# Kernel optimization log

Measured on AMD Instinct MI355X. Metric: run time of the kernel, lower is better.

## Reference

```python
import jax, jax.numpy as jnp
import numpy as np


def _gcn_conv(x, W, b, row, col, norm, n_nodes):
    # x: [N, Fin]; W: [Fin, Fout]. PyG GCNConv: linear -> normalized gather/scatter-add -> +bias
    h = x @ W                                   # [N, Fout]
    msgs = h[row] * norm[:, None]               # [E+N, Fout] gather + scale
    out = jax.ops.segment_sum(msgs, col, num_segments=n_nodes)  # scatter-add
    return out + b


def _gcn_norm(edge_index, n_nodes):
    # add self-loops, then sym-normalize: deg^{-1/2}[row] * deg^{-1/2}[col]
    loops = jnp.arange(n_nodes, dtype=edge_index.dtype)
    row = jnp.concatenate([edge_index[0], loops])
    col = jnp.concatenate([edge_index[1], loops])
    ones = jnp.ones(row.shape[0], dtype=jnp.float32)
    deg = jax.ops.segment_sum(ones, col, num_segments=n_nodes)
    dinv = jnp.where(deg > 0, jax.lax.rsqrt(deg), 0.0)
    norm = dinv[row] * dinv[col]
    return row, col, norm


def setup_inputs() -> dict:
    key = jax.random.key(0)
    k1, k2, k3, k4 = jax.random.split(key, 4)
    N, E, F, H, C = 100000, 1600000, 256, 128, 40
    x = jax.random.normal(k1, (N, F), dtype=jnp.float32)
    edge_index = jax.random.randint(k2, (2, E), 0, N, dtype=jnp.int64)
    W1 = jax.random.normal(k3, (F, H), dtype=jnp.float32) * (1.0 / np.sqrt(F))
    b1 = jnp.zeros((H,), dtype=jnp.float32)
    W2 = jax.random.normal(k4, (H, C), dtype=jnp.float32) * (1.0 / np.sqrt(H))
    b2 = jnp.zeros((C,), dtype=jnp.float32)
    return {"x": x, "edge_index": edge_index, "W1": W1, "b1": b1, "W2": W2, "b2": b2}


def reference(x, edge_index, W1, b1, W2, b2):
    n_nodes = x.shape[0]
    row, col, norm = _gcn_norm(edge_index, n_nodes)
    h = _gcn_conv(x, W1, b1, row, col, norm, n_nodes)
    h = jax.nn.relu(h)
    # F.dropout in eval mode is identity (reference run deterministically)
    h = _gcn_conv(h, W2, b2, row, col, norm, n_nodes)
    return jax.nn.log_softmax(h, axis=1)
```

## Files before the change

kernel.cpp:

```cpp
#include <hip/hip_runtime.h>
#include <hip/hip_bf16.h>
#include <math.h>
#include <stdint.h>

typedef unsigned short u16;
typedef unsigned int u32;
typedef __attribute__((ext_vector_type(8))) short short8;
typedef __attribute__((ext_vector_type(4))) float f32x4;
typedef __attribute__((ext_vector_type(2))) float f32x2;

#define BN 256
#define NBMAX 400
#define EPB 4096
#define ST1 160
#define ST2 192

__device__ __forceinline__ u16 bfbits(float f) {
    __hip_bfloat16 h = __float2bfloat16(f);
    return *reinterpret_cast<u16*>(&h);
}
__device__ __forceinline__ float bflo(u32 v) { return __uint_as_float(v << 16); }
__device__ __forceinline__ float bfhi(u32 v) { return __uint_as_float(v & 0xffff0000u); }

template <bool HI>
__device__ __forceinline__ f32x2 fp8pair(u32 v) {
#if __has_builtin(__builtin_amdgcn_cvt_pk_f32_fp8)
    return __builtin_amdgcn_cvt_pk_f32_fp8(v, HI);
#else
    f32x2 r;
    r.x = __builtin_amdgcn_cvt_f32_fp8(v, HI ? 2 : 0);
    r.y = __builtin_amdgcn_cvt_f32_fp8(v, HI ? 3 : 1);
    return r;
#endif
}

__device__ __forceinline__ int sigma128(int col) {
    int a = col >> 6, c = (col >> 4) & 3, lr = col & 15;
    return (a << 6) + (lr << 2) + c;
}

__global__ __launch_bounds__(256) void k_pre(const int* __restrict__ ei, int E, int n, int nb,
                                             int nblkc, int* __restrict__ gcnt,
                                             const float* __restrict__ w1, short* __restrict__ w1bf,
                                             const float* __restrict__ b1, const float* __restrict__ w2,
                                             float* __restrict__ b1p, float* __restrict__ w2p) {
    __shared__ int sh[NBMAX];
    const int t = threadIdx.x;
    const int b = blockIdx.x;
    if (b < nblkc) {
        const int* col = ei + E;
        for (int i = t; i < nb; i += 256) sh[i] = 0;
        __syncthreads();
        const int base = b * EPB;
#pragma unroll
        for (int j = 0; j < 16; ++j) {
            int e = base + j * 256 + t;
            if (e < E) {
                unsigned c = (unsigned)col[e];
                if (c < (unsigned)n) atomicAdd(&sh[c >> 8], 1);
            }
        }
        __syncthreads();
        for (int i = t; i < nb; i += 256)
            if (sh[i]) atomicAdd(&gcnt[i], sh[i]);
    } else if (b < nblkc + 128) {
        int i = (b - nblkc) * 256 + t;
        int e = i & 7, l = (i >> 3) & 63, kt = (i >> 9) & 7, ct = i >> 12;
        int k = kt * 32 + (l >> 4) * 8 + e;
        int c = ct * 16 + (l & 15);
        w1bf[i] = (short)bfbits(w1[(size_t)k * 128 + c]);
    } else {
        int i = (b - nblkc - 128) * 256 + t;
        if (i < 128) b1p[sigma128(i)] = b1[i];
        int j = i - 128;
        if (j >= 0 && j < 128 * 40) {
            int col = j / 40, jj = j - col * 40;
            w2p[sigma128(col) * 40 + jj] = w2[j];
        }
    }
}

__global__ __launch_bounds__(512) void k_bscan(const int* __restrict__ gcnt,
                                               int* __restrict__ ebase, int* __restrict__ cursor,
                                               int* __restrict__ off, int nb, int n) {
    __shared__ int sh[512];
    const int t = threadIdx.x;
    int v = (t < nb) ? gcnt[t] : 0;
    sh[t] = v;
    __syncthreads();
    for (int d = 1; d < 512; d <<= 1) {
        int x = (t >= d) ? sh[t - d] : 0;
        __syncthreads();
        sh[t] += x;
        __syncthreads();
    }
    if (t < nb) {
        int excl = sh[t] - v;
        ebase[t] = excl;
        cursor[t] = excl;
    }
    if (t == 0) {
        ebase[nb] = sh[511];
        off[n] = sh[511] + n;
    }
}

struct SMemScat { int cnt[NBMAX]; int cbase[NBMAX]; };
union SMemU {
    SMemScat s;
    u16 xt[64 * 128];
};

__global__ __launch_bounds__(256) void k_scatg1(const int* __restrict__ ei,
                                                int* __restrict__ cursor, u32* __restrict__ staging,
                                                int E, int n, int nb, int nblks,
                                                const float* __restrict__ x,
                                                const short* __restrict__ w1bf,
                                                u32* __restrict__ hbf8) {
    __shared__ SMemU sm;
    const int t = threadIdx.x;
    if ((int)blockIdx.x < nblks) {
        for (int i = t; i < nb; i += 256) sm.s.cnt[i] = 0;
        __syncthreads();
        const int base = blockIdx.x * EPB;
        int rr[16], cc[16], rk[16];
#pragma unroll
        for (int j = 0; j < 16; ++j) {
            int e = base + j * 256 + t;
            cc[j] = -1;
            if (e < E) {
                unsigned r = (unsigned)ei[e], c = (unsigned)ei[E + e];
                if (r < (unsigned)n && c < (unsigned)n) {
                    rr[j] = (int)r;
                    cc[j] = (int)c;
                    rk[j] = atomicAdd(&sm.s.cnt[c >> 8], 1);
                }
            }
        }
        __syncthreads();
        for (int i = t; i < nb; i += 256)
            if (sm.s.cnt[i]) sm.s.cbase[i] = atomicAdd(&cursor[i], sm.s.cnt[i]);
        __syncthreads();
#pragma unroll
        for (int j = 0; j < 16; ++j) {
            if (cc[j] >= 0) {
                int b = cc[j] >> 8;
                staging[sm.s.cbase[b] + rk[j]] = (u32)rr[j] | ((u32)(cc[j] & (BN - 1)) << 17);
            }
        }
        return;
    }
    const int bid = blockIdx.x - nblks;
    const int wv = t >> 6, l = t & 63;
    const int mrow = wv >> 1, mcol = wv & 1;
    const int lr = l & 15, kg = l >> 4;
    const int n0 = bid * 64;

    const short* bbase = w1bf + ((size_t)(4 * mcol) * 8) * 64 * 8 + (size_t)l * 8;

    f32x4 zero = {0.f, 0.f, 0.f, 0.f};
    f32x4 acc[2][4];
#pragma unroll
    for (int m = 0; m < 2; ++m)
#pragma unroll
        for (int c = 0; c < 4; ++c) acc[m][c] = zero;

#pragma unroll
    for (int p = 0; p < 2; ++p) {
        __syncthreads();
#pragma unroll
        for (int j = 0; j < 8; ++j) {
            int idx = j * 256 + t;
            int row = idx >> 5;
            int kf4 = idx & 31;
            int grow = n0 + row;
            if (grow > n - 1) grow = n - 1;
            float4 v = *(const float4*)(x + (size_t)grow * 256 + p * 128 + kf4 * 4);
            u32 w0 = (u32)bfbits(v.x) | ((u32)bfbits(v.y) << 16);
            u32 w1v = (u32)bfbits(v.z) | ((u32)bfbits(v.w) << 16);
            int bir = kf4 * 8;
            int sb = row * 256 + (bir ^ ((row & 7) << 4));
            *(uint2*)((char*)sm.xt + sb) = make_uint2(w0, w1v);
        }
        __syncthreads();
#pragma unroll
        for (int ktl = 0; ktl < 4; ++ktl) {
            int kt = p * 4 + ktl;
            short8 af[2];
#pragma unroll
            for (int m = 0; m < 2; ++m) {
                int r = 32 * mrow + 16 * m + lr;
                int bir = ktl * 64 + kg * 16;
                int sb = r * 256 + (bir ^ ((r & 7) << 4));
                af[m] = *(const short8*)((const char*)sm.xt + sb);
            }
#pragma unroll
            for (int c = 0; c < 4; ++c) {
                short8 bfrag = *(const short8*)(bbase + ((size_t)(c * 8 + kt) * 64) * 8);
#pragma unroll
                for (int m = 0; m < 2; ++m)
                    acc[m][c] = __builtin_amdgcn_mfma_f32_16x16x32_bf16(af[m], bfrag,
                                                                        acc[m][c], 0, 0, 0);
            }
        }
    }

#pragma unroll
    for (int m = 0; m < 2; ++m) {
        int rbase = n0 + 32 * mrow + 16 * m + kg * 4;
#pragma unroll
        for (int r = 0; r < 4; ++r) {
            int row = rbase + r;
            if (row < n) {
                int w = __builtin_amdgcn_cvt_pk_fp8_f32(acc[m][0][r], acc[m][1][r], 0, false);
                w = __builtin_amdgcn_cvt_pk_fp8_f32(acc[m][2][r], acc[m][3][r], w, true);
                hbf8[(size_t)row * 32 + 16 * mcol + lr] = (u32)w;
            }
        }
    }
}

__global__ __launch_bounds__(256) void k_build(const u32* __restrict__ staging,
                                               const int* __restrict__ ebase,
                                               int* __restrict__ csrs, int* __restrict__ off,
                                               float* __restrict__ dinv, int n) {
    __shared__ int sh[256];
    __shared__ int cur[256];
    const int t = threadIdx.x;
    const int b = blockIdx.x;
    const int e0 = ebase[b], e1 = ebase[b + 1];
    const int node0 = b * BN;
    const int nn = min(BN, n - node0);
    sh[t] = 0;
    __syncthreads();
    for (int i = e0 + t; i < e1; i += 256)
        atomicAdd(&sh[staging[i] >> 17], 1);
    __syncthreads();
    const int mycnt = sh[t];
    const int myval = (t < nn) ? mycnt + 1 : 0;
    sh[t] = myval;
    __syncthreads();
    for (int d = 1; d < 256; d <<= 1) {
        int x = (t >= d) ? sh[t - d] : 0;
        __syncthreads();
        sh[t] += x;
        __syncthreads();
    }
    const int excl = sh[t] - myval;
    const int csrbase = e0 + node0;
    if (t < nn) {
        int node = node0 + t;
        int o = csrbase + excl;
        off[node] = o;
        dinv[node] = rsqrtf((float)(mycnt + 1));
        csrs[o] = node;
        cur[t] = o + 1;
    }
    __syncthreads();
    for (int i = e0 + t; i < e1; i += 256) {
        u32 v = staging[i];
        int p = atomicAdd(&cur[v >> 17], 1);
        csrs[p] = (int)(v & 0x1FFFF);
    }
}

__global__ __launch_bounds__(256) void k_agg1(const u32* __restrict__ hbf8,
                                              const int* __restrict__ off,
                                              const int* __restrict__ csrs,
                                              const float* __restrict__ dinv,
                                              const float* __restrict__ b1p,
                                              u16* __restrict__ h1b, int n) {
    __shared__ int s_s[8][ST1];
    __shared__ float s_f[8][ST1];
    const int t = threadIdx.x, h = t >> 5, fl = t & 31;
    const int node = blockIdx.x * 8 + h;
    const int nd = node < n ? node : n - 1;
    const float dn = dinv[nd];
    const int e0 = off[nd], e1 = off[nd + 1];
    const int deg = e1 - e0;
    const int nst = deg < ST1 ? deg : ST1;
    for (int i = fl; i < nst; i += 32) {
        int s = csrs[e0 + i];
        s_s[h][i] = s;
        s_f[h][i] = dinv[s] * dn;
    }
    __syncthreads();

    const int onst = __shfl_xor(nst, 32, 64);
    const int nmin = nst < onst ? nst : onst;
    const int nmax = nst > onst ? nst : onst;
    const int odeg = __shfl_xor(deg, 32, 64);
    const int dmax = deg > odeg ? deg : odeg;

    const u32* hb = hbf8;
    float a0 = 0.f, a1 = 0.f, a2 = 0.f, a3 = 0.f;
    int i = 0;
    for (; i + 16 <= nmin; i += 16) {
        u32 vv[16];
        float ww[16];
#pragma unroll
        for (int k = 0; k < 16; ++k) {
            int s = s_s[h][i + k];
            ww[k] = s_f[h][i + k];
            vv[k] = hb[(size_t)s * 32 + fl];
        }
#pragma unroll
        for (int k = 0; k < 16; ++k) {
            f32x2 lo = fp8pair<false>(vv[k]), hi = fp8pair<true>(vv[k]);
            a0 = fmaf(lo.x, ww[k], a0); a1 = fmaf(lo.y, ww[k], a1);
            a2 = fmaf(hi.x, ww[k], a2); a3 = fmaf(hi.y, ww[k], a3);
        }
    }
    for (; i + 4 <= nmin; i += 4) {
        u32 vv[4];
        float ww[4];
#pragma unroll
        for (int k = 0; k < 4; ++k) {
            int s = s_s[h][i + k];
            ww[k] = s_f[h][i + k];
            vv[k] = hb[(size_t)s * 32 + fl];
        }
#pragma unroll
        for (int k = 0; k < 4; ++k) {
            f32x2 lo = fp8pair<false>(vv[k]), hi = fp8pair<true>(vv[k]);
            a0 = fmaf(lo.x, ww[k], a0); a1 = fmaf(lo.y, ww[k], a1);
            a2 = fmaf(hi.x, ww[k], a2); a3 = fmaf(hi.y, ww[k], a3);
        }
    }
    for (; i < nmin; ++i) {
        int s = s_s[h][i];
        float w = s_f[h][i];
        u32 v = hb[(size_t)s * 32 + fl];
        f32x2 lo = fp8pair<false>(v), hi = fp8pair<true>(v);
        a0 = fmaf(lo.x, w, a0); a1 = fmaf(lo.y, w, a1);
        a2 = fmaf(hi.x, w, a2); a3 = fmaf(hi.y, w, a3);
    }
    for (; i < nmax; ++i) {
        bool ok = i < nst;
        int s = ok ? s_s[h][i] : nd;
        float w = ok ? s_f[h][i] : 0.f;
        u32 v = hb[(size_t)s * 32 + fl];
        f32x2 lo = fp8pair<false>(v), hi = fp8pair<true>(v);
        a0 = fmaf(lo.x, w, a0); a1 = fmaf(lo.y, w, a1);
        a2 = fmaf(hi.x, w, a2); a3 = fmaf(hi.y, w, a3);
    }
    for (int j = ST1; j < dmax; ++j) {
        bool ok = j < deg;
        int s = ok ? csrs[e0 + j] : nd;
        float w = ok ? dinv[s] * dn : 0.f;
        u32 v = hb[(size_t)s * 32 + fl];
        f32x2 lo = fp8pair<false>(v), hi = fp8pair<true>(v);
        a0 = fmaf(lo.x, w, a0); a1 = fmaf(lo.y, w, a1);
        a2 = fmaf(hi.x, w, a2); a3 = fmaf(hi.y, w, a3);
    }

    float4 bb = *(const float4*)(b1p + 4 * fl);
    float r0 = fmaxf(a0 + bb.x, 0.f);
    float r1 = fmaxf(a1 + bb.y, 0.f);
    float r2 = fmaxf(a2 + bb.z, 0.f);
    float r3 = fmaxf(a3 + bb.w, 0.f);
    if (node < n) {
        uint2 o;
        o.x = (u32)bfbits(r0) | ((u32)bfbits(r1) << 16);
        o.y = (u32)bfbits(r2) | ((u32)bfbits(r3) << 16);
        ((uint2*)h1b)[(size_t)node * 32 + fl] = o;
    }
}

__global__ __launch_bounds__(64) void k_gemm2(const u16* __restrict__ h1b,
                                              const float* __restrict__ w2p,
                                              u32* __restrict__ h2q, float* __restrict__ scl,
                                              int n) {
    __shared__ float hs[64 * 132];
    const int t = threadIdx.x;
    const int n0 = blockIdx.x * 64;
    const uint4* src = (const uint4*)(h1b + (size_t)n0 * 128);
#pragma unroll
    for (int i = 0; i < 16; ++i) {
        int idx = i * 64 + t;
        int r = idx >> 4, q = idx & 15;
        uint4 v = make_uint4(0u, 0u, 0u, 0u);
        if (n0 + r < n) v = src[(size_t)r * 16 + q];
        *(float4*)&hs[r * 132 + q * 8] =
            make_float4(bflo(v.x), bfhi(v.x), bflo(v.y), bfhi(v.y));
        *(float4*)&hs[r * 132 + q * 8 + 4] =
            make_float4(bflo(v.z), bfhi(v.z), bflo(v.w), bfhi(v.w));
    }
    __syncthreads();

    float acc[40];
#pragma unroll
    for (int c = 0; c < 40; ++c) acc[c] = 0.f;

    for (int k4 = 0; k4 < 32; ++k4) {
        float4 hv = *(const float4*)&hs[t * 132 + 4 * k4];
#pragma unroll
        for (int j = 0; j < 4; ++j) {
            float xv = (j == 0) ? hv.x : (j == 1) ? hv.y : (j == 2) ? hv.z : hv.w;
            const float* wr = w2p + (size_t)(4 * k4 + j) * 40;
#pragma unroll
            for (int c = 0; c < 40; ++c) acc[c] = fmaf(xv, wr[c], acc[c]);
        }
    }
    __syncthreads();

    float mx = 0.f;
#pragma unroll
    for (int c = 0; c < 40; ++c) mx = fmaxf(mx, fabsf(acc[c]));
    const float qs = mx > 0.f ? 127.f / mx : 0.f;
    u32* rowp = (u32*)hs + t * 16;
#pragma unroll
    for (int j = 0; j < 10; ++j) {
        u32 w = 0;
#pragma unroll
        for (int k = 0; k < 4; ++k) {
            int q = __float2int_rn(acc[4 * j + k] * qs);
            q = q > 127 ? 127 : (q < -127 ? -127 : q);
            w |= ((u32)(q & 255)) << (8 * k);
        }
        rowp[j] = w;
    }
#pragma unroll
    for (int j = 10; j < 16; ++j) rowp[j] = 0;
    __syncthreads();
    const int nrow = (n - n0 < 64) ? n - n0 : 64;
    uint4* dst = (uint4*)(h2q + (size_t)n0 * 16);
    const uint4* s4 = (const uint4*)hs;
#pragma unroll
    for (int i = 0; i < 4; ++i) {
        int idx = i * 64 + t;
        if ((idx >> 2) < nrow) dst[idx] = s4[idx];
    }
    if (t < nrow) scl[n0 + t] = mx * (1.f / 127.f);
}

__global__ __launch_bounds__(256) void k_agg2(const u32* __restrict__ h2q,
                                              const float* __restrict__ scl,
                                              const int* __restrict__ off,
                                              const int* __restrict__ csrs,
                                              const float* __restrict__ dinv,
                                              const float* __restrict__ b2,
                                              float* __restrict__ out, int n) {
    __shared__ int s_s[4][ST2];
    __shared__ float s_f[4][ST2];
    const int t = threadIdx.x, wv = t >> 6, l = t & 63;
    const int node = blockIdx.x * 4 + wv;
    const int nd = node < n ? node : n - 1;
    const float dn = dinv[nd];
    const int e0 = off[nd], e1 = off[nd + 1];
    const int deg = e1 - e0;
    const int nst = deg < ST2 ? deg : ST2;
    for (int i = l; i < nst; i += 64) {
        int s = csrs[e0 + i];
        s_s[wv][i] = s;
        s_f[wv][i] = dinv[s] * dn * scl[s];
    }
    __syncthreads();

    const int g = l >> 4;
    const int fl = l & 15;

#define ACC4(v, w)                                                         \
    {                                                                      \
        a0 = fmaf((float)(int)(signed char)((v) & 0xff), (w), a0);         \
        a1 = fmaf((float)(int)(signed char)(((v) >> 8) & 0xff), (w), a1);  \
        a2 = fmaf((float)(int)(signed char)(((v) >> 16) & 0xff), (w), a2); \
        a3 = fmaf((float)(int)(signed char)((v) >> 24), (w), a3);          \
    }

    float a0 = 0.f, a1 = 0.f, a2 = 0.f, a3 = 0.f;
    int base = 0;
    for (; base + 16 <= nst; base += 16) {
        int eA = base + g, eB = base + 4 + g, eC = base + 8 + g, eD = base + 12 + g;
        int sA = s_s[wv][eA], sB = s_s[wv][eB], sC = s_s[wv][eC], sD = s_s[wv][eD];
        float wA = s_f[wv][eA], wB = s_f[wv][eB], wC = s_f[wv][eC], wD = s_f[wv][eD];
        u32 vA = h2q[(size_t)sA * 16 + fl];
        u32 vB = h2q[(size_t)sB * 16 + fl];
        u32 vC = h2q[(size_t)sC * 16 + fl];
        u32 vD = h2q[(size_t)sD * 16 + fl];
        ACC4(vA, wA); ACC4(vB, wB); ACC4(vC, wC); ACC4(vD, wD);
    }
    for (; base < nst; base += 4) {
        int e = base + g;
        bool ok = e < nst;
        int s = ok ? s_s[wv][e] : nd;
        float w = ok ? s_f[wv][e] : 0.f;
        u32 v = h2q[(size_t)s * 16 + fl];
        ACC4(v, w);
    }
    for (int j = nst; j < deg; j += 4) {
        int e = j + g;
        bool ok = e < deg;
        int s = ok ? csrs[e0 + e] : nd;
        float w = ok ? dinv[s] * dn * scl[s] : 0.f;
        u32 v = h2q[(size_t)s * 16 + fl];
        ACC4(v, w);
    }
#undef ACC4

    float t0 = __shfl(a0, (l + 32) & 63, 64);
    float t1 = __shfl(a1, (l + 32) & 63, 64);
    float t2 = __shfl(a2, (l + 32) & 63, 64);
    float t3 = __shfl(a3, (l + 32) & 63, 64);
    a0 += t0; a1 += t1; a2 += t2; a3 += t3;
    t0 = __shfl(a0, (l + 16) & 63, 64);
    t1 = __shfl(a1, (l + 16) & 63, 64);
    t2 = __shfl(a2, (l + 16) & 63, 64);
    t3 = __shfl(a3, (l + 16) & 63, 64);
    a0 += t0; a1 += t1; a2 += t2; a3 += t3;

    const bool act = (l < 10);
    float4 bb = *(const float4*)(b2 + 4 * (act ? l : 9));
    float v0 = a0 + bb.x, v1 = a1 + bb.y, v2 = a2 + bb.z, v3 = a3 + bb.w;

    float m = act ? fmaxf(fmaxf(v0, v1), fmaxf(v2, v3)) : -INFINITY;
#pragma unroll
    for (int d = 8; d > 0; d >>= 1) m = fmaxf(m, __shfl_xor(m, d, 16));
    float s = act ? (__expf(v0 - m) + __expf(v1 - m) + __expf(v2 - m) + __expf(v3 - m)) : 0.f;
#pragma unroll
    for (int d = 8; d > 0; d >>= 1) s += __shfl_xor(s, d, 16);
    float ls = logf(s);
    if (node < n && act) {
        float4 o = make_float4(v0 - m - ls, v1 - m - ls, v2 - m - ls, v3 - m - ls);
        *(float4*)(out + (size_t)node * 40 + 4 * l) = o;
    }
}

extern "C" void kernel_launch(void* const* d_in, const int* in_sizes, int n_in,
                              void* d_out, int out_size, void* d_ws, size_t ws_size,
                              hipStream_t stream) {
    const float* x = (const float*)d_in[0];
    const int* ei = (const int*)d_in[1];
    const float* w1 = (const float*)d_in[2];
    const float* b1 = (const float*)d_in[3];
    const float* w2 = (const float*)d_in[4];
    const float* b2 = (const float*)d_in[5];
    float* out = (float*)d_out;

    const int N = in_sizes[0] / 256;
    const int E = in_sizes[1] / 2;
    const int NB = (N + BN - 1) / BN;

    char* p = (char*)d_ws;
    auto alloc = [&](size_t bytes) {
        char* r = p;
        p += (bytes + 255) & ~(size_t)255;
        return r;
    };
    int* gcnt = (int*)alloc((size_t)NB * 4);
    int* ebase = (int*)alloc((size_t)(NB + 1) * 4);
    int* cursor = (int*)alloc((size_t)NB * 4);
    int* off = (int*)alloc((size_t)(N + 1) * 4);
    float* dinv = (float*)alloc((size_t)N * 4);
    float* scl = (float*)alloc((size_t)N * 4);
    int* csrs = (int*)alloc((size_t)(E + N) * 4);
    short* w1bf = (short*)alloc(32768 * 2);
    float* b1p = (float*)alloc(128 * 4);
    float* w2p = (float*)alloc(128 * 40 * 4);
    u32* hbf8 = (u32*)alloc((size_t)N * 32 * 4);
    u16* h1b = (u16*)alloc((size_t)N * 128 * 2);
    u32* staging = (u32*)h1b;
    u32* h2q = hbf8;

    const int nblk = (E + EPB - 1) / EPB;
    const int g1blk = (N + 63) / 64;

    (void)hipMemsetAsync(gcnt, 0, (size_t)NB * 4, stream);
    k_pre<<<nblk + 128 + 21, 256, 0, stream>>>(ei, E, N, NB, nblk, gcnt, w1, w1bf,
                                               b1, w2, b1p, w2p);
    k_bscan<<<1, 512, 0, stream>>>(gcnt, ebase, cursor, off, NB, N);
    k_scatg1<<<nblk + g1blk, 256, 0, stream>>>(ei, cursor, staging, E, N, NB, nblk,
                                               x, w1bf, hbf8);
    k_build<<<NB, 256, 0, stream>>>(staging, ebase, csrs, off, dinv, N);
    k_agg1<<<(N + 7) / 8, 256, 0, stream>>>(hbf8, off, csrs, dinv, b1p, h1b, N);
    k_gemm2<<<g1blk, 64, 0, stream>>>(h1b, w2p, h2q, scl, N);
    k_agg2<<<(N + 3) / 4, 256, 0, stream>>>(h2q, scl, off, csrs, dinv, b2, out, N);
}
```

Measured before the change: 237.5 us.

## Fuse second-layer GEMM and int8 quantization into first aggregation kernel

```diff
diff --git a/kernel.cpp b/kernel.cpp
--- a/kernel.cpp
+++ b/kernel.cpp
@@ -12,7 +12,7 @@
 #define BN 256
 #define NBMAX 400
 #define EPB 4096
-#define ST1 160
+#define ST1 152
 #define ST2 192
 
 __device__ __forceinline__ u16 bfbits(float f) {
@@ -43,7 +43,7 @@
                                              int nblkc, int* __restrict__ gcnt,
                                              const float* __restrict__ w1, short* __restrict__ w1bf,
                                              const float* __restrict__ b1, const float* __restrict__ w2,
-                                             float* __restrict__ b1p, float* __restrict__ w2p) {
+                                             float* __restrict__ b1p, float* __restrict__ w2t) {
     __shared__ int sh[NBMAX];
     const int t = threadIdx.x;
     const int b = blockIdx.x;
@@ -74,8 +74,8 @@
         if (i < 128) b1p[sigma128(i)] = b1[i];
         int j = i - 128;
         if (j >= 0 && j < 128 * 40) {
-            int col = j / 40, jj = j - col * 40;
-            w2p[sigma128(col) * 40 + jj] = w2[j];
+            int k = j / 40, c = j - k * 40;
+            w2t[(size_t)c * 128 + sigma128(k)] = w2[j];
         }
     }
 }
@@ -264,14 +264,23 @@
     }
 }
 
-__global__ __launch_bounds__(256) void k_agg1(const u32* __restrict__ hbf8,
-                                              const int* __restrict__ off,
-                                              const int* __restrict__ csrs,
-                                              const float* __restrict__ dinv,
-                                              const float* __restrict__ b1p,
-                                              u16* __restrict__ h1b, int n) {
-    __shared__ int s_s[8][ST1];
-    __shared__ float s_f[8][ST1];
+struct AggH {
+    union {
+        struct { int s[ST1]; float f[ST1]; } g;
+        struct { float h1[128]; float out[48]; } e;
+    };
+    int pad[16];
+};
+
+__global__ __launch_bounds__(256) void k_agg1g2(const u32* __restrict__ hbf8,
+                                                const int* __restrict__ off,
+                                                const int* __restrict__ csrs,
+                                                const float* __restrict__ dinv,
+                                                const float* __restrict__ b1p,
+                                                const float* __restrict__ w2t,
+                                                u32* __restrict__ h2q, float* __restrict__ scl,
+                                                int n) {
+    __shared__ AggH sm[8];
     const int t = threadIdx.x, h = t >> 5, fl = t & 31;
     const int node = blockIdx.x * 8 + h;
     const int nd = node < n ? node : n - 1;
@@ -281,8 +290,8 @@
     const int nst = deg < ST1 ? deg : ST1;
     for (int i = fl; i < nst; i += 32) {
         int s = csrs[e0 + i];
-        s_s[h][i] = s;
-        s_f[h][i] = dinv[s] * dn;
+        sm[h].g.s[i] = s;
+        sm[h].g.f[i] = dinv[s] * dn;
     }
     __syncthreads();
 
@@ -300,8 +309,8 @@
         float ww[16];
 #pragma unroll
         for (int k = 0; k < 16; ++k) {
-            int s = s_s[h][i + k];
-            ww[k] = s_f[h][i + k];
+            int s = sm[h].g.s[i + k];
+            ww[k] = sm[h].g.f[i + k];
             vv[k] = hb[(size_t)s * 32 + fl];
         }
 #pragma unroll
@@ -316,8 +325,8 @@
         float ww[4];
 #pragma unroll
         for (int k = 0; k < 4; ++k) {
-            int s = s_s[h][i + k];
-            ww[k] = s_f[h][i + k];
+            int s = sm[h].g.s[i + k];
+            ww[k] = sm[h].g.f[i + k];
             vv[k] = hb[(size_t)s * 32 + fl];
         }
 #pragma unroll
@@ -328,8 +337,8 @@
         }
     }
     for (; i < nmin; ++i) {
-        int s = s_s[h][i];
-        float w = s_f[h][i];
+        int s = sm[h].g.s[i];
+        float w = sm[h].g.f[i];
         u32 v = hb[(size_t)s * 32 + fl];
         f32x2 lo = fp8pair<false>(v), hi = fp8pair<true>(v);
         a0 = fmaf(lo.x, w, a0); a1 = fmaf(lo.y, w, a1);
@@ -337,8 +346,8 @@
     }
     for (; i < nmax; ++i) {
         bool ok = i < nst;
-        int s = ok ? s_s[h][i] : nd;
-        float w = ok ? s_f[h][i] : 0.f;
+        int s = ok ? sm[h].g.s[i] : nd;
+        float w = ok ? sm[h].g.f[i] : 0.f;
         u32 v = hb[(size_t)s * 32 + fl];
         f32x2 lo = fp8pair<false>(v), hi = fp8pair<true>(v);
         a0 = fmaf(lo.x, w, a0); a1 = fmaf(lo.y, w, a1);
@@ -359,79 +368,47 @@
     float r1 = fmaxf(a1 + bb.y, 0.f);
     float r2 = fmaxf(a2 + bb.z, 0.f);
     float r3 = fmaxf(a3 + bb.w, 0.f);
+    *(float4*)&sm[h].e.h1[4 * fl] = make_float4(r0, r1, r2, r3);
+
+    const int c2 = (fl < 8) ? 32 + fl : 39;
+    const float* w2r1 = w2t + (size_t)fl * 128;
+    const float* w2r2 = w2t + (size_t)c2 * 128;
+    float acc1 = 0.f, acc2 = 0.f;
+#pragma unroll
+    for (int kk = 0; kk < 32; ++kk) {
+        float4 hv = *(const float4*)&sm[h].e.h1[4 * kk];
+        float4 wa = *(const float4*)(w2r1 + 4 * kk);
+        float4 wb = *(const float4*)(w2r2 + 4 * kk);
+        acc1 = fmaf(hv.x, wa.x, acc1); acc1 = fmaf(hv.y, wa.y, acc1);
+        acc1 = fmaf(hv.z, wa.z, acc1); acc1 = fmaf(hv.w, wa.w, acc1);
+        acc2 = fmaf(hv.x, wb.x, acc2); acc2 = fmaf(hv.y, wb.y, acc2);
+        acc2 = fmaf(hv.z, wb.z, acc2); acc2 = fmaf(hv.w, wb.w, acc2);
+    }
+    sm[h].e.out[fl] = acc1;
+    if (fl < 8) sm[h].e.out[32 + fl] = acc2;
+
+    float m = fabsf(acc1);
+    if (fl < 8) m = fmaxf(m, fabsf(acc2));
+#pragma unroll
+    for (int d = 16; d > 0; d >>= 1) m = fmaxf(m, __shfl_xor(m, d, 32));
+    const float qs = m > 0.f ? 127.f / m : 0.f;
+
     if (node < n) {
-        uint2 o;
-        o.x = (u32)bfbits(r0) | ((u32)bfbits(r1) << 16);
-        o.y = (u32)bfbits(r2) | ((u32)bfbits(r3) << 16);
-        ((uint2*)h1b)[(size_t)node * 32 + fl] = o;
-    }
-}
-
-__global__ __launch_bounds__(64) void k_gemm2(const u16* __restrict__ h1b,
-                                              const float* __restrict__ w2p,
-                                              u32* __restrict__ h2q, float* __restrict__ scl,
-                                              int n) {
-    __shared__ float hs[64 * 132];
-    const int t = threadIdx.x;
-    const int n0 = blockIdx.x * 64;
-    const uint4* src = (const uint4*)(h1b + (size_t)n0 * 128);
-#pragma unroll
-    for (int i = 0; i < 16; ++i) {
-        int idx = i * 64 + t;
-        int r = idx >> 4, q = idx & 15;
-        uint4 v = make_uint4(0u, 0u, 0u, 0u);
-        if (n0 + r < n) v = src[(size_t)r * 16 + q];
-        *(float4*)&hs[r * 132 + q * 8] =
-            make_float4(bflo(v.x), bfhi(v.x), bflo(v.y), bfhi(v.y));
-        *(float4*)&hs[r * 132 + q * 8 + 4] =
-            make_float4(bflo(v.z), bfhi(v.z), bflo(v.w), bfhi(v.w));
-    }
-    __syncthreads();
-
-    float acc[40];
-#pragma unroll
-    for (int c = 0; c < 40; ++c) acc[c] = 0.f;
-
-    for (int k4 = 0; k4 < 32; ++k4) {
-        float4 hv = *(const float4*)&hs[t * 132 + 4 * k4];
-#pragma unroll
-        for (int j = 0; j < 4; ++j) {
-            float xv = (j == 0) ? hv.x : (j == 1) ? hv.y : (j == 2) ? hv.z : hv.w;
-            const float* wr = w2p + (size_t)(4 * k4 + j) * 40;
-#pragma unroll
-            for (int c = 0; c < 40; ++c) acc[c] = fmaf(xv, wr[c], acc[c]);
-        }
-    }
-    __syncthreads();
-
-    float mx = 0.f;
-#pragma unroll
-    for (int c = 0; c < 40; ++c) mx = fmaxf(mx, fabsf(acc[c]));
-    const float qs = mx > 0.f ? 127.f / mx : 0.f;
-    u32* rowp = (u32*)hs + t * 16;
-#pragma unroll
-    for (int j = 0; j < 10; ++j) {
-        u32 w = 0;
-#pragma unroll
-        for (int k = 0; k < 4; ++k) {
-            int q = __float2int_rn(acc[4 * j + k] * qs);
-            q = q > 127 ? 127 : (q < -127 ? -127 : q);
-            w |= ((u32)(q & 255)) << (8 * k);
-        }
-        rowp[j] = w;
-    }
-#pragma unroll
-    for (int j = 10; j < 16; ++j) rowp[j] = 0;
-    __syncthreads();
-    const int nrow = (n - n0 < 64) ? n - n0 : 64;
-    uint4* dst = (uint4*)(h2q + (size_t)n0 * 16);
-    const uint4* s4 = (const uint4*)hs;
-#pragma unroll
-    for (int i = 0; i < 4; ++i) {
-        int idx = i * 64 + t;
-        if ((idx >> 2) < nrow) dst[idx] = s4[idx];
-    }
-    if (t < nrow) scl[n0 + t] = mx * (1.f / 127.f);
+        if (fl < 16) {
+            u32 w = 0;
+            if (fl < 10) {
+#pragma unroll
+                for (int k = 0; k < 4; ++k) {
+                    float v = sm[h].e.out[4 * fl + k];
+                    int q = __float2int_rn(v * qs);
+                    q = q > 127 ? 127 : (q < -127 ? -127 : q);
+                    w |= ((u32)(q & 255)) << (8 * k);
+                }
+            }
+            h2q[(size_t)node * 16 + fl] = w;
+        }
+        if (fl == 0) scl[node] = m * (1.f / 127.f);
+    }
 }
 
 __global__ __launch_bounds__(256) void k_agg2(const u32* __restrict__ h2q,
@@ -556,23 +533,23 @@
     int* csrs = (int*)alloc((size_t)(E + N) * 4);
     short* w1bf = (short*)alloc(32768 * 2);
     float* b1p = (float*)alloc(128 * 4);
-    float* w2p = (float*)alloc(128 * 40 * 4);
+    float* w2t = (float*)alloc(40 * 128 * 4);
     u32* hbf8 = (u32*)alloc((size_t)N * 32 * 4);
-    u16* h1b = (u16*)alloc((size_t)N * 128 * 2);
-    u32* staging = (u32*)h1b;
+    u32* staging = (u32*)alloc((size_t)(E + N) * 4);
     u32* h2q = hbf8;
+    h2q = (u32*)alloc((size_t)N * 16 * 4);
 
     const int nblk = (E + EPB - 1) / EPB;
     const int g1blk = (N + 63) / 64;
 
     (void)hipMemsetAsync(gcnt, 0, (size_t)NB * 4, stream);
     k_pre<<<nblk + 128 + 21, 256, 0, stream>>>(ei, E, N, NB, nblk, gcnt, w1, w1bf,
-                                               b1, w2, b1p, w2p);
+                                               b1, w2, b1p, w2t);
     k_bscan<<<1, 512, 0, stream>>>(gcnt, ebase, cursor, off, NB, N);
     k_scatg1<<<nblk + g1blk, 256, 0, stream>>>(ei, cursor, staging, E, N, NB, nblk,
                                                x, w1bf, hbf8);
     k_build<<<NB, 256, 0, stream>>>(staging, ebase, csrs, off, dinv, N);
-    k_agg1<<<(N + 7) / 8, 256, 0, stream>>>(hbf8, off, csrs, dinv, b1p, h1b, N);
-    k_gemm2<<<g1blk, 64, 0, stream>>>(h1b, w2p, h2q, scl, N);
+    k_agg1g2<<<(N + 7) / 8, 256, 0, stream>>>(hbf8, off, csrs, dinv, b1p, w2t,
+                                              h2q, scl, N);
     k_agg2<<<(N + 3) / 4, 256, 0, stream>>>(h2q, scl, off, csrs, dinv, b2, out, N);
 }
```

After: 395.8 us. 66.7% more time.
